# Kernel optimization log

Hardware: AMD Instinct MI355X
Metric: run time of the kernel (lower is better)

Reference implementation:

```python
import jax, jax.numpy as jnp
import numpy as np

N = 100000
E = 1600000
HEADS = 4
OUT_C = 32
IN_C = 128
NEG_SLOPE = 0.2
EPS = 1e-16


def setup_inputs() -> dict:
    key = jax.random.key(0)
    ks = jax.random.split(key, 6)
    x = jax.random.normal(ks[0], (N, IN_C), dtype=jnp.float32)
    edge_index = jax.random.randint(ks[1], (2, E), 0, N, dtype=jnp.int32)
    # Glorot-ish scaled params (scale only affects magnitudes, not the math)
    W = jax.random.normal(ks[2], (IN_C, HEADS * OUT_C), dtype=jnp.float32) * (1.0 / np.sqrt(IN_C))
    att_src = jax.random.normal(ks[3], (HEADS, OUT_C), dtype=jnp.float32) * (1.0 / np.sqrt(OUT_C))
    att_dst = jax.random.normal(ks[4], (HEADS, OUT_C), dtype=jnp.float32) * (1.0 / np.sqrt(OUT_C))
    bias = jnp.zeros((HEADS * OUT_C,), dtype=jnp.float32)
    return {"x": x, "edge_index": edge_index, "W": W, "att_src": att_src, "att_dst": att_dst, "bias": bias}


def reference(x, edge_index, W, att_src, att_dst, bias):
    n = x.shape[0]
    heads, out_c = att_src.shape
    # add self loops (PyG add_self_loops=True): append edges (i, i)
    loop = jnp.arange(n, dtype=edge_index.dtype)
    src = jnp.concatenate([edge_index[0], loop])  # source j
    dst = jnp.concatenate([edge_index[1], loop])  # target i

    # linear projection: [n, heads, out_c]
    h = (x @ W).reshape(n, heads, out_c)

    # per-node attention logits: [n, heads]
    a_src = jnp.einsum('nhc,hc->nh', h, att_src)
    a_dst = jnp.einsum('nhc,hc->nh', h, att_dst)

    # per-edge score with LeakyReLU: [e, heads]
    e = a_src[src] + a_dst[dst]
    e = jnp.where(e >= 0, e, NEG_SLOPE * e)

    # segment softmax over incoming edges per target node
    m = jax.ops.segment_max(e, dst, num_segments=n)          # [n, heads]
    m = jnp.where(jnp.isfinite(m), m, 0.0)                   # nodes with no in-edges
    ex = jnp.exp(e - m[dst])
    s = jax.ops.segment_sum(ex, dst, num_segments=n)         # [n, heads]
    alpha = ex / (s[dst] + EPS)                              # [e, heads]

    # weighted scatter-aggregate of source features
    msg = h[src] * alpha[:, :, None]                         # [e, heads, out_c]
    out = jax.ops.segment_sum(msg, dst, num_segments=n)      # [n, heads, out_c]
    return out.reshape(n, heads * out_c) + bias
```

## Files before the change

### kernel.cpp

```cpp
#include <hip/hip_runtime.h>
#include <hip/hip_fp16.h>

#define NEG_SLOPE 0.2f
#define EPS 1e-16f
#define MAXNB 512
#define BSHIFT 8
#define BNODES 256
#define CHUNK 8192
#define CAPR 6144
#define CAPC 8192
#define GB 512

typedef _Float16 f16x8 __attribute__((ext_vector_type(8)));
typedef float    f32x4 __attribute__((ext_vector_type(4)));

__global__ __launch_bounds__(256) void gemm_mfma(const float* __restrict__ x,
                                                 const float* __restrict__ W,
                                                 const float* __restrict__ att_src,
                                                 const float* __restrict__ att_dst,
                                                 __half* __restrict__ h16,
                                                 float* __restrict__ a_src,
                                                 float* __restrict__ a_dst, int N) {
    __shared__ _Float16 ldsT[4][16][264];
    __shared__ float atts[4][33];
    __shared__ float attd[4][33];
    for (int i = threadIdx.x; i < 128; i += 256) {
        atts[i >> 5][i & 31] = att_src[i];
        attd[i >> 5][i & 31] = att_dst[i];
    }
    __syncthreads();
    const int lane = threadIdx.x & 63;
    const int wid  = threadIdx.x >> 6;
    const int q    = lane >> 4;
    const int t    = lane & 15;
    f16x8 bfrag[8][4];
#pragma unroll
    for (int ct = 0; ct < 8; ++ct)
#pragma unroll
        for (int kt = 0; kt < 4; ++kt) {
            const float* wp = W + (size_t)(kt * 32 + q * 8) * 128 + ct * 16 + t;
            f16x8 b;
#pragma unroll
            for (int j = 0; j < 8; ++j) b[j] = (_Float16)wp[(size_t)j * 128];
            bfrag[ct][kt] = b;
        }
    const int lrow = lane >> 2;
    const int lhd  = lane & 3;
    const int strips = (N + 15) >> 4;
    for (int s = blockIdx.x * 4 + wid; s < strips; s += GB * 4) {
        int row0 = s << 4;
        int row  = row0 + t;
        const float* xp = x + (size_t)((row < N) ? row : (N - 1)) * 128;
        f16x8 afrag[4];
#pragma unroll
        for (int kt = 0; kt < 4; ++kt) {
            float4 u0 = *(const float4*)(xp + kt * 32 + q * 8);
            float4 u1 = *(const float4*)(xp + kt * 32 + q * 8 + 4);
            f16x8 a;
            a[0] = (_Float16)u0.x; a[1] = (_Float16)u0.y;
            a[2] = (_Float16)u0.z; a[3] = (_Float16)u0.w;
            a[4] = (_Float16)u1.x; a[5] = (_Float16)u1.y;
            a[6] = (_Float16)u1.z; a[7] = (_Float16)u1.w;
            afrag[kt] = a;
        }
        f32x4 acc[8];
#pragma unroll
        for (int ct = 0; ct < 8; ++ct) acc[ct] = (f32x4){0.f, 0.f, 0.f, 0.f};
#pragma unroll
        for (int kt = 0; kt < 4; ++kt)
#pragma unroll
            for (int ct = 0; ct < 8; ++ct)
                acc[ct] = __builtin_amdgcn_mfma_f32_16x16x32_f16(afrag[kt], bfrag[ct][kt],
                                                                 acc[ct], 0, 0, 0);
#pragma unroll
        for (int ct = 0; ct < 8; ++ct)
#pragma unroll
            for (int r = 0; r < 4; ++r)
                ldsT[wid][q * 4 + r][ct * 16 + t] = (_Float16)acc[ct][r];
        float4 raw[4];
#pragma unroll
        for (int j = 0; j < 4; ++j)
            raw[j] = *(const float4*)&ldsT[wid][lrow][lhd * 32 + j * 8];
        int orow = row0 + lrow;
        if (orow < N) {
            float4* gp = (float4*)(h16 + (size_t)orow * 128 + lhd * 32);
            gp[0] = raw[0]; gp[1] = raw[1]; gp[2] = raw[2]; gp[3] = raw[3];
            const __half2* hv = (const __half2*)raw;
            float s1 = 0.f, s2 = 0.f;
#pragma unroll
            for (int c = 0; c < 16; ++c) {
                float2 f = __half22float2(hv[c]);
                s1 = fmaf(f.x, atts[lhd][2 * c], s1);
                s1 = fmaf(f.y, atts[lhd][2 * c + 1], s1);
                s2 = fmaf(f.x, attd[lhd][2 * c], s2);
                s2 = fmaf(f.y, attd[lhd][2 * c + 1], s2);
            }
            a_src[orow * 4 + lhd] = s1;
            a_dst[orow * 4 + lhd] = s2;
        }
    }
}

__global__ __launch_bounds__(256) void binA(const int* __restrict__ ei,
                                            int* __restrict__ gcursor,
                                            unsigned* __restrict__ records,
                                            int E, int N) {
    __shared__ unsigned stage[CHUNK];
    __shared__ unsigned short bkt[CHUNK];
    __shared__ int lhist[MAXNB];
    __shared__ int lbase[MAXNB];
    int T = E + N;
    int c0 = blockIdx.x * CHUNK;
    for (int i = threadIdx.x; i < MAXNB; i += 256) lhist[i] = 0;
    __syncthreads();
    int cnt = min(CHUNK, T - c0);
    for (int i = threadIdx.x; i < cnt; i += 256) {
        int e = c0 + i;
        int src, dst;
        if (e < E) { src = ei[e]; dst = ei[E + e]; }
        else       { src = dst = e - E; }
        int b = dst >> BSHIFT;
        stage[i] = ((unsigned)(dst & (BNODES - 1)) << 17) | (unsigned)src;
        bkt[i]   = (unsigned short)b;
        atomicAdd(&lhist[b], 1);
    }
    __syncthreads();
    for (int b = threadIdx.x; b < MAXNB; b += 256) {
        int h = lhist[b];
        lbase[b] = h ? (b * CAPR + atomicAdd(&gcursor[b], h)) : 0;
    }
    __syncthreads();
    for (int i = threadIdx.x; i < cnt; i += 256) {
        int b = bkt[i];
        int pos = atomicAdd(&lbase[b], 1);
        records[pos] = stage[i];
    }
}

__global__ __launch_bounds__(512, 8) void aggr_fused(const unsigned* __restrict__ records,
                                                     const int* __restrict__ gcursor,
                                                     const float* __restrict__ a_src,
                                                     const float* __restrict__ a_dst,
                                                     const __half* __restrict__ h16,
                                                     const float* __restrict__ bias,
                                                     float* __restrict__ out, int N) {
    __shared__ int lcsr[CAPC];
    __shared__ int ncnt[BNODES];
    __shared__ int nbeg[BNODES];
    __shared__ int relcur[BNODES];
    __shared__ int psum[BNODES];
    int b = blockIdx.x;
    int node0 = b << BSHIFT;
    int nn = min(BNODES, N - node0);
    int t = threadIdx.x;
    if (t < BNODES) ncnt[t] = 0;
    __syncthreads();
    int rbase = b * CAPR;
    int cntb  = gcursor[b];
    for (int r = t; r < cntb; r += 512)
        atomicAdd(&ncnt[records[rbase + r] >> 17], 1);
    __syncthreads();
    int va = 0, vap = 0;
    if (t < BNODES) { va = ncnt[t]; vap = (va + 7) & ~7; psum[t] = vap; }
    __syncthreads();
    for (int off = 1; off < BNODES; off <<= 1) {
        int y = 0;
        if (t < BNODES && t >= off) y = psum[t - off];
        __syncthreads();
        if (t < BNODES) psum[t] += y;
        __syncthreads();
    }
    if (t < BNODES) {
        int ex = psum[t] - vap;
        nbeg[t]   = ex;
        relcur[t] = ex;
    }
    __syncthreads();
    for (int r = t; r < cntb; r += 512) {
        unsigned rec = records[rbase + r];
        int pos = atomicAdd(&relcur[rec >> 17], 1);
        lcsr[pos] = rec & 0x1FFFF;
    }
    __syncthreads();
    int lane = t & 15;
    int ln   = t >> 4;
    int hd   = lane >> 2;
    int c0   = lane * 8;
    for (int pass = 0; pass < BNODES / 32; ++pass) {
        int nl = pass * 32 + ln;
        if (nl >= nn) continue;
        int node = node0 + nl;
        float ad = a_dst[node * 4 + hd];
        int beg  = nbeg[nl];
        int cnt  = ncnt[nl];
        float acc[8];
#pragma unroll
        for (int j = 0; j < 8; ++j) acc[j] = 0.f;
        float den = 0.f;
        int k = 0;
        for (; k + 4 <= cnt; k += 4) {
            int bb = beg + k;
            int s0 = lcsr[bb], s1 = lcsr[bb + 1], s2 = lcsr[bb + 2], s3 = lcsr[bb + 3];
            float e0 = a_src[s0 * 4 + hd];
            float e1 = a_src[s1 * 4 + hd];
            float e2 = a_src[s2 * 4 + hd];
            float e3 = a_src[s3 * 4 + hd];
            float4 g0 = *(const float4*)(h16 + (size_t)s0 * 128 + c0);
            float4 g1 = *(const float4*)(h16 + (size_t)s1 * 128 + c0);
            float4 g2 = *(const float4*)(h16 + (size_t)s2 * 128 + c0);
            float4 g3 = *(const float4*)(h16 + (size_t)s3 * 128 + c0);
            float sc;
            sc = e0 + ad; sc = (sc >= 0.f) ? sc : NEG_SLOPE * sc; float w0 = __expf(sc);
            sc = e1 + ad; sc = (sc >= 0.f) ? sc : NEG_SLOPE * sc; float w1 = __expf(sc);
            sc = e2 + ad; sc = (sc >= 0.f) ? sc : NEG_SLOPE * sc; float w2 = __expf(sc);
            sc = e3 + ad; sc = (sc >= 0.f) ? sc : NEG_SLOPE * sc; float w3 = __expf(sc);
            den += w0 + w1 + w2 + w3;
            const __half2* p0 = (const __half2*)&g0;
            const __half2* p1 = (const __half2*)&g1;
            const __half2* p2 = (const __half2*)&g2;
            const __half2* p3 = (const __half2*)&g3;
#pragma unroll
            for (int j = 0; j < 4; ++j) {
                float2 f0 = __half22float2(p0[j]);
                float2 f1 = __half22float2(p1[j]);
                float2 f2 = __half22float2(p2[j]);
                float2 f3 = __half22float2(p3[j]);
                acc[2 * j]     = fmaf(w0, f0.x, acc[2 * j]);
                acc[2 * j + 1] = fmaf(w0, f0.y, acc[2 * j + 1]);
                acc[2 * j]     = fmaf(w1, f1.x, acc[2 * j]);
                acc[2 * j + 1] = fmaf(w1, f1.y, acc[2 * j + 1]);
                acc[2 * j]     = fmaf(w2, f2.x, acc[2 * j]);
                acc[2 * j + 1] = fmaf(w2, f2.y, acc[2 * j + 1]);
                acc[2 * j]     = fmaf(w3, f3.x, acc[2 * j]);
                acc[2 * j + 1] = fmaf(w3, f3.y, acc[2 * j + 1]);
            }
        }
        for (; k < cnt; ++k) {
            int s = lcsr[beg + k];
            float e0 = a_src[s * 4 + hd];
            float4 g = *(const float4*)(h16 + (size_t)s * 128 + c0);
            float sc = e0 + ad; sc = (sc >= 0.f) ? sc : NEG_SLOPE * sc;
            float w = __expf(sc);
            den += w;
            const __half2* p = (const __half2*)&g;
#pragma unroll
            for (int j = 0; j < 4; ++j) {
                float2 f = __half22float2(p[j]);
                acc[2 * j]     = fmaf(w, f.x, acc[2 * j]);
                acc[2 * j + 1] = fmaf(w, f.y, acc[2 * j + 1]);
            }
        }
        float inv = 1.f / (den + EPS);
        float4 o0, o1;
        o0.x = fmaf(acc[0], inv, bias[c0]);
        o0.y = fmaf(acc[1], inv, bias[c0 + 1]);
        o0.z = fmaf(acc[2], inv, bias[c0 + 2]);
        o0.w = fmaf(acc[3], inv, bias[c0 + 3]);
        o1.x = fmaf(acc[4], inv, bias[c0 + 4]);
        o1.y = fmaf(acc[5], inv, bias[c0 + 5]);
        o1.z = fmaf(acc[6], inv, bias[c0 + 6]);
        o1.w = fmaf(acc[7], inv, bias[c0 + 7]);
        float* op = out + (size_t)node * 128 + c0;
        *(float4*)op       = o0;
        *(float4*)(op + 4) = o1;
    }
}

extern "C" void kernel_launch(void* const* d_in, const int* in_sizes, int n_in,
                              void* d_out, int out_size, void* d_ws, size_t ws_size,
                              hipStream_t stream) {
    const float* x       = (const float*)d_in[0];
    const int*   ei      = (const int*)  d_in[1];
    const float* W       = (const float*)d_in[2];
    const float* att_src = (const float*)d_in[3];
    const float* att_dst = (const float*)d_in[4];
    const float* bias    = (const float*)d_in[5];
    float*       out     = (float*)d_out;

    const int N  = in_sizes[0] / 128;
    const int E  = in_sizes[1] / 2;
    const int T  = E + N;
    const int NB = (N + BNODES - 1) >> BSHIFT;

    __half*   h16     = (__half*)d_ws;
    float*    a_src   = (float*)(h16 + (size_t)N * 128);
    float*    a_dst   = a_src + (size_t)N * 4;
    int*      gcursor = (int*)(a_dst + (size_t)N * 4);
    unsigned* records = (unsigned*)(gcursor + MAXNB);

    (void)hipMemsetAsync(gcursor, 0, MAXNB * sizeof(int), stream);

    gemm_mfma<<<GB, 256, 0, stream>>>(x, W, att_src, att_dst, h16, a_src, a_dst, N);

    binA<<<(T + CHUNK - 1) / CHUNK, 256, 0, stream>>>(ei, gcursor, records, E, N);

    aggr_fused<<<NB, 512, 0, stream>>>(records, gcursor, a_src, a_dst, h16, bias, out, N);
}
```

Baseline: 230.4 us.

## Merge GEMM and edge binning into one launch and halve bucket size

Combines the MFMA projection kernel and the edge-binning kernel into a single grid, where the first GB blocks do the GEMM and the rest bin edges, sharing LDS through a union. This lets the two independent stages run at the same time and removes one launch. Bucket size drops from 256 to 128 nodes, with smaller chunk and capacity values, so the aggregation kernel gets twice as many blocks. The trade-off is more global cursor atomics and smaller per-bucket capacity margins, which could overflow on skewed degree distributions.

Result: slower. 236.2 us (+2.5%).

```diff
diff --git a/kernel.cpp b/kernel.cpp
--- a/kernel.cpp
+++ b/kernel.cpp
@@ -3,30 +3,77 @@
 
 #define NEG_SLOPE 0.2f
 #define EPS 1e-16f
-#define MAXNB 512
-#define BSHIFT 8
-#define BNODES 256
-#define CHUNK 8192
-#define CAPR 6144
-#define CAPC 8192
+#define MAXNB 1024
+#define BSHIFT 7
+#define BNODES 128
+#define CHUNK 4096
+#define CAPR 3072
+#define CAPC 4096
 #define GB 512
 
 typedef _Float16 f16x8 __attribute__((ext_vector_type(8)));
 typedef float    f32x4 __attribute__((ext_vector_type(4)));
 
-__global__ __launch_bounds__(256) void gemm_mfma(const float* __restrict__ x,
+struct GemmSmem {
+    _Float16 ldsT[4][16][264];
+    float atts[4][33];
+    float attd[4][33];
+};
+struct BinASmem {
+    unsigned stage[CHUNK];
+    unsigned short bkt[CHUNK];
+    int lhist[MAXNB];
+    int lbase[MAXNB];
+};
+union SmemU {
+    GemmSmem g;
+    BinASmem a;
+};
+
+__global__ __launch_bounds__(256) void gemm_binA(const float* __restrict__ x,
                                                  const float* __restrict__ W,
                                                  const float* __restrict__ att_src,
                                                  const float* __restrict__ att_dst,
+                                                 const int* __restrict__ ei,
+                                                 int* __restrict__ gcursor,
+                                                 unsigned* __restrict__ records,
                                                  __half* __restrict__ h16,
                                                  float* __restrict__ a_src,
-                                                 float* __restrict__ a_dst, int N) {
-    __shared__ _Float16 ldsT[4][16][264];
-    __shared__ float atts[4][33];
-    __shared__ float attd[4][33];
+                                                 float* __restrict__ a_dst,
+                                                 int N, int E) {
+    __shared__ SmemU sh;
+    if (blockIdx.x >= GB) {
+        int T = E + N;
+        int c0 = (int)(blockIdx.x - GB) * CHUNK;
+        for (int i = threadIdx.x; i < MAXNB; i += 256) sh.a.lhist[i] = 0;
+        __syncthreads();
+        int cnt = min(CHUNK, T - c0);
+        for (int i = threadIdx.x; i < cnt; i += 256) {
+            int e = c0 + i;
+            int src, dst;
+            if (e < E) { src = ei[e]; dst = ei[E + e]; }
+            else       { src = dst = e - E; }
+            int b = dst >> BSHIFT;
+            sh.a.stage[i] = ((unsigned)(dst & (BNODES - 1)) << 17) | (unsigned)src;
+            sh.a.bkt[i]   = (unsigned short)b;
+            atomicAdd(&sh.a.lhist[b], 1);
+        }
+        __syncthreads();
+        for (int b = threadIdx.x; b < MAXNB; b += 256) {
+            int h = sh.a.lhist[b];
+            sh.a.lbase[b] = h ? (b * CAPR + atomicAdd(&gcursor[b], h)) : 0;
+        }
+        __syncthreads();
+        for (int i = threadIdx.x; i < cnt; i += 256) {
+            int b = sh.a.bkt[i];
+            int pos = atomicAdd(&sh.a.lbase[b], 1);
+            records[pos] = sh.a.stage[i];
+        }
+        return;
+    }
     for (int i = threadIdx.x; i < 128; i += 256) {
-        atts[i >> 5][i & 31] = att_src[i];
-        attd[i >> 5][i & 31] = att_dst[i];
+        sh.g.atts[i >> 5][i & 31] = att_src[i];
+        sh.g.attd[i >> 5][i & 31] = att_dst[i];
     }
     __syncthreads();
     const int lane = threadIdx.x & 63;
@@ -76,11 +123,11 @@
         for (int ct = 0; ct < 8; ++ct)
 #pragma unroll
             for (int r = 0; r < 4; ++r)
-                ldsT[wid][q * 4 + r][ct * 16 + t] = (_Float16)acc[ct][r];
+                sh.g.ldsT[wid][q * 4 + r][ct * 16 + t] = (_Float16)acc[ct][r];
         float4 raw[4];
 #pragma unroll
         for (int j = 0; j < 4; ++j)
-            raw[j] = *(const float4*)&ldsT[wid][lrow][lhd * 32 + j * 8];
+            raw[j] = *(const float4*)&sh.g.ldsT[wid][lrow][lhd * 32 + j * 8];
         int orow = row0 + lrow;
         if (orow < N) {
             float4* gp = (float4*)(h16 + (size_t)orow * 128 + lhd * 32);
@@ -90,50 +137,14 @@
 #pragma unroll
             for (int c = 0; c < 16; ++c) {
                 float2 f = __half22float2(hv[c]);
-                s1 = fmaf(f.x, atts[lhd][2 * c], s1);
-                s1 = fmaf(f.y, atts[lhd][2 * c + 1], s1);
-                s2 = fmaf(f.x, attd[lhd][2 * c], s2);
-                s2 = fmaf(f.y, attd[lhd][2 * c + 1], s2);
+                s1 = fmaf(f.x, sh.g.atts[lhd][2 * c], s1);
+                s1 = fmaf(f.y, sh.g.atts[lhd][2 * c + 1], s1);
+                s2 = fmaf(f.x, sh.g.attd[lhd][2 * c], s2);
+                s2 = fmaf(f.y, sh.g.attd[lhd][2 * c + 1], s2);
             }
             a_src[orow * 4 + lhd] = s1;
             a_dst[orow * 4 + lhd] = s2;
         }
-    }
-}
-
-__global__ __launch_bounds__(256) void binA(const int* __restrict__ ei,
-                                            int* __restrict__ gcursor,
-                                            unsigned* __restrict__ records,
-                                            int E, int N) {
-    __shared__ unsigned stage[CHUNK];
-    __shared__ unsigned short bkt[CHUNK];
-    __shared__ int lhist[MAXNB];
-    __shared__ int lbase[MAXNB];
-    int T = E + N;
-    int c0 = blockIdx.x * CHUNK;
-    for (int i = threadIdx.x; i < MAXNB; i += 256) lhist[i] = 0;
-    __syncthreads();
-    int cnt = min(CHUNK, T - c0);
-    for (int i = threadIdx.x; i < cnt; i += 256) {
-        int e = c0 + i;
-        int src, dst;
-        if (e < E) { src = ei[e]; dst = ei[E + e]; }
-        else       { src = dst = e - E; }
-        int b = dst >> BSHIFT;
-        stage[i] = ((unsigned)(dst & (BNODES - 1)) << 17) | (unsigned)src;
-        bkt[i]   = (unsigned short)b;
-        atomicAdd(&lhist[b], 1);
-    }
-    __syncthreads();
-    for (int b = threadIdx.x; b < MAXNB; b += 256) {
-        int h = lhist[b];
-        lbase[b] = h ? (b * CAPR + atomicAdd(&gcursor[b], h)) : 0;
-    }
-    __syncthreads();
-    for (int i = threadIdx.x; i < cnt; i += 256) {
-        int b = bkt[i];
-        int pos = atomicAdd(&lbase[b], 1);
-        records[pos] = stage[i];
     }
 }
 
@@ -277,10 +288,11 @@
     const float* bias    = (const float*)d_in[5];
     float*       out     = (float*)d_out;
 
-    const int N  = in_sizes[0] / 128;
-    const int E  = in_sizes[1] / 2;
-    const int T  = E + N;
-    const int NB = (N + BNODES - 1) >> BSHIFT;
+    const int N     = in_sizes[0] / 128;
+    const int E     = in_sizes[1] / 2;
+    const int T     = E + N;
+    const int NB    = (N + BNODES - 1) >> BSHIFT;
+    const int NBINA = (T + CHUNK - 1) / CHUNK;
 
     __half*   h16     = (__half*)d_ws;
     float*    a_src   = (float*)(h16 + (size_t)N * 128);
@@ -290,9 +302,8 @@
 
     (void)hipMemsetAsync(gcursor, 0, MAXNB * sizeof(int), stream);
 
-    gemm_mfma<<<GB, 256, 0, stream>>>(x, W, att_src, att_dst, h16, a_src, a_dst, N);
-
-    binA<<<(T + CHUNK - 1) / CHUNK, 256, 0, stream>>>(ei, gcursor, records, E, N);
+    gemm_binA<<<GB + NBINA, 256, 0, stream>>>(x, W, att_src, att_dst, ei, gcursor,
+                                              records, h16, a_src, a_dst, N, E);
 
     aggr_fused<<<NB, 512, 0, stream>>>(records, gcursor, a_src, a_dst, h16, bias, out, N);
 }
```
